# Kernel tuning notes

Measured on AMD Instinct MI355X. Metric: run time of the kernel, lower is better.

## Reference

```python
import jax, jax.numpy as jnp
import numpy as np

N, F, E, B, D = 100000, 256, 128, 10000, 32
GAMMA, ZETA = -0.1, 1.1  # hard-concrete stretch params of L0Dense


def setup_inputs() -> dict:
    key = jax.random.key(0)
    ks = jax.random.split(key, 12)
    return {
        "nodes": jax.random.randint(ks[0], (B,), 0, N),
        "neigh_idx": jax.random.randint(ks[1], (B, D), 0, N),
        "neigh_mask": jax.random.bernoulli(ks[2], 0.9, (B, D)),
        "feature": jax.random.normal(ks[3], (N, F), jnp.float32),
        "W": jax.random.normal(ks[4], (F, E), jnp.float32) * 0.05,
        "b": jnp.zeros((E,), jnp.float32),
        "qz_loga": jax.random.normal(ks[5], (F,), jnp.float32),
        "att1_w": jax.random.normal(ks[6], (2 * E, E), jnp.float32) * 0.05,
        "att1_b": jnp.zeros((E,), jnp.float32),
        "att2_w": jax.random.normal(ks[7], (E, E), jnp.float32) * 0.05,
        "att2_b": jnp.zeros((E,), jnp.float32),
        "att3_w": jax.random.normal(ks[8], (E, 1), jnp.float32) * 0.05,
        "att3_b": jnp.zeros((1,), jnp.float32),
    }


def reference(nodes, neigh_idx, neigh_mask, feature, W, b, qz_loga,
              att1_w, att1_b, att2_w, att2_b, att3_w, att3_b):
    # L0Dense, deterministic (eval) hard-concrete gate on input dims
    z = jnp.clip(jax.nn.sigmoid(qz_loga) * (ZETA - GAMMA) + GAMMA, 0.0, 1.0)
    We = W * z[:, None]                                  # [F, E]

    node_feat = feature[nodes] @ We + b                   # [B, E]
    neigh_feat = feature[neigh_idx] @ We + b              # [B, D, E]

    # GraphRec-style attention MLP over (neighbor, center) pairs
    h = jnp.concatenate(
        [neigh_feat, jnp.broadcast_to(node_feat[:, None, :], neigh_feat.shape)],
        axis=-1)                                          # [B, D, 2E]
    h = jax.nn.relu(h @ att1_w + att1_b)
    h = jax.nn.relu(h @ att2_w + att2_b)
    scores = (h @ att3_w + att3_b)[..., 0]                # [B, D]
    scores = jnp.where(neigh_mask, scores, -1e30)
    att = jax.nn.softmax(scores, axis=-1)                 # [B, D]

    agg = jnp.einsum('bd,bde->be', att, neigh_feat)       # weighted sum
    has_neigh = neigh_mask.any(axis=-1, keepdims=True)
    return jnp.where(has_neigh, agg, node_feat)           # n==0 fallback
```

## Files before the change

### kernel.cpp

```cpp
#include <hip/hip_runtime.h>
#include <hip/hip_bf16.h>
#include <math.h>

#define NN 100000
#define FF 256
#define EE 128
#define BB_ 10000
#define DD 32

typedef __attribute__((ext_vector_type(8))) short short8;
typedef __attribute__((ext_vector_type(4))) float f32x4;

__device__ __forceinline__ short f2bf(float f) {
  __hip_bfloat16 h = __float2bfloat16(f);
  union { __hip_bfloat16 h; short s; } u; u.h = h;
  return u.s;
}
__device__ __forceinline__ float bf2f(short s) {
  union { unsigned u; float f; } v;
  v.u = ((unsigned)(unsigned short)s) << 16;
  return v.f;
}

__device__ __forceinline__ void gll16(const float* g, float* lds) {
  __builtin_amdgcn_global_load_lds(
      (const __attribute__((address_space(1))) unsigned int*)g,
      (__attribute__((address_space(3))) unsigned int*)lds, 16, 0, 0);
}

__global__ __launch_bounds__(256) void k_prep(
    const float* __restrict__ W, const float* __restrict__ qz,
    const float* __restrict__ a1w, const float* __restrict__ a2w,
    const float* __restrict__ bb,
    float* __restrict__ Wef32, short* __restrict__ BT2,
    short* __restrict__ a1wTc, short* __restrict__ w2T,
    float* __restrict__ bias2) {
  int i = blockIdx.x * 256 + threadIdx.x;
  if (i < 32768) {
    int f = i >> 7, e = i & 127;
    float g = qz[f];
    float s = 1.0f / (1.0f + expf(-g));
    float z = fminf(fmaxf(s * 1.2f - 0.1f, 0.0f), 1.0f);
    float v = W[f * 128 + e] * z;
    Wef32[f * 128 + e] = v;
    BT2[e * 256 + f] = f2bf(v);
  } else if (i < 49152) {
    int t = i - 32768; int n = t >> 7, k = t & 127;
    a1wTc[n * 128 + k] = f2bf(a1w[(128 + k) * 128 + n]);
  } else if (i < 65536) {
    int t = i - 49152; int n = t >> 7, k = t & 127;
    w2T[n * 128 + k] = f2bf(a2w[k * 128 + n]);
  } else if (i < 65664) {
    bias2[i - 65536] = bb[i - 65536];
  }
}

__global__ __launch_bounds__(256) void k_compose(
    const float* __restrict__ Wef32, const float* __restrict__ a1w,
    const float* __restrict__ a1b, const float* __restrict__ bb,
    short* __restrict__ BT2, float* __restrict__ bias2) {
  const int n = blockIdx.x;
  const int f = threadIdx.x;
  float s = 0.f;
  for (int e = 0; e < 128; ++e)
    s = fmaf(a1w[e * 128 + n], Wef32[f * 128 + e], s);
  BT2[(size_t)(128 + n) * 256 + f] = f2bf(s);
  if (f == 0) {
    float by = a1b[n];
    for (int e = 0; e < 128; ++e) by = fmaf(bb[e], a1w[e * 128 + n], by);
    bias2[128 + n] = by;
  }
}

__global__ __launch_bounds__(256) void k_xy(
    const float* __restrict__ feat, const short* __restrict__ BT2,
    const float* __restrict__ bias2, short* __restrict__ XY, int M) {
  __shared__ float As[2][32 * 256];
  const int tid = threadIdx.x;
  const int wave = tid >> 6, lane = tid & 63;
  const int wn = wave;
  const int l15 = lane & 15, lg = lane >> 4;
  const int NT = M >> 5;
  const int G = gridDim.x;

  short8 bfr[8][4];
#pragma unroll
  for (int ks = 0; ks < 8; ++ks)
#pragma unroll
    for (int j = 0; j < 4; ++j)
      bfr[ks][j] = *(const short8*)(BT2 +
          (size_t)(wn * 64 + j * 16 + l15) * 256 + (ks * 4 + lg) * 8);
  float bv4[4];
#pragma unroll
  for (int j = 0; j < 4; ++j) bv4[j] = bias2[wn * 64 + j * 16 + l15];

  int t = blockIdx.x;
  if (t < NT) {
#pragma unroll
    for (int it = 0; it < 8; ++it) {
      int r = it * 4 + wave;
      gll16(feat + (size_t)(t * 32 + r) * 256 + ((lane ^ (r & 7)) * 4),
            &As[0][r * 256]);
    }
  }

  int cur = 0;
  for (; t < NT; t += G) {
    const int tn = t + G;
    __builtin_amdgcn_s_barrier();
    if (tn < NT) {
#pragma unroll
      for (int it = 0; it < 8; ++it) {
        int r = it * 4 + wave;
        gll16(feat + (size_t)(tn * 32 + r) * 256 + ((lane ^ (r & 7)) * 4),
              &As[cur ^ 1][r * 256]);
      }
      asm volatile("s_waitcnt vmcnt(8)" ::: "memory");
    } else {
      asm volatile("s_waitcnt vmcnt(0)" ::: "memory");
    }
    __builtin_amdgcn_s_barrier();
    __builtin_amdgcn_sched_barrier(0);

    f32x4 acc[2][4];
#pragma unroll
    for (int i = 0; i < 2; ++i)
#pragma unroll
      for (int j = 0; j < 4; ++j) acc[i][j] = (f32x4){0.f, 0.f, 0.f, 0.f};

    const float* Ab = &As[cur][0];
#pragma unroll
    for (int ks = 0; ks < 8; ++ks) {
      const int kg = ks * 4 + lg;
#pragma unroll
      for (int i = 0; i < 2; ++i) {
        const int r = i * 16 + l15;
        const int sw = r & 7;
        const int c0 = (2 * kg) ^ sw;
        const int c1 = (2 * kg + 1) ^ sw;
        float4 flo = *(const float4*)(Ab + r * 256 + c0 * 4);
        float4 fhi = *(const float4*)(Ab + r * 256 + c1 * 4);
        short8 af;
        af[0] = f2bf(flo.x); af[1] = f2bf(flo.y);
        af[2] = f2bf(flo.z); af[3] = f2bf(flo.w);
        af[4] = f2bf(fhi.x); af[5] = f2bf(fhi.y);
        af[6] = f2bf(fhi.z); af[7] = f2bf(fhi.w);
        __builtin_amdgcn_s_setprio(1);
#pragma unroll
        for (int j = 0; j < 4; ++j)
          acc[i][j] = __builtin_amdgcn_mfma_f32_16x16x32_bf16(
              af, bfr[ks][j], acc[i][j], 0, 0, 0);
        __builtin_amdgcn_s_setprio(0);
      }
    }

#pragma unroll
    for (int i = 0; i < 2; ++i) {
#pragma unroll
      for (int r = 0; r < 4; ++r) {
        int row = t * 32 + i * 16 + lg * 4 + r;
#pragma unroll
        for (int j = 0; j < 4; ++j) {
          int col = wn * 64 + j * 16 + l15;
          XY[(size_t)row * 256 + col] = f2bf(acc[i][j][r] + bv4[j]);
        }
      }
    }
    cur ^= 1;
  }
}

template <int K, int LDA, int LDC, bool AF32, bool OUTBF16>
__global__ __launch_bounds__(256) void k_mm(
    const void* __restrict__ Ap, const short* __restrict__ BT,
    const float* __restrict__ bias, const int* __restrict__ idx,
    void* __restrict__ Cp, int M) {
  __shared__ short As[128 * 64];
  __shared__ short Bs[128 * 64];
  const int tid = threadIdx.x;
  const int mb = blockIdx.x * 128;
  const int col0 = blockIdx.y * 128;
  const int wave = tid >> 6, lane = tid & 63;
  const int wr = wave >> 1, wc = wave & 1;
  const int l15 = lane & 15, lg = lane >> 4;

  size_t abase[4];
#pragma unroll
  for (int s = 0; s < 4; ++s) {
    int row = (tid + s * 256) >> 3;
    int grow = mb + row;
    int gr = 0;
    if (grow < M) gr = idx ? idx[grow] : grow;
    abase[s] = (size_t)gr * LDA;
  }

  f32x4 acc[4][4];
#pragma unroll
  for (int i = 0; i < 4; ++i)
#pragma unroll
    for (int j = 0; j < 4; ++j) acc[i][j] = (f32x4){0.f, 0.f, 0.f, 0.f};

  for (int k0 = 0; k0 < K; k0 += 64) {
#pragma unroll
    for (int s = 0; s < 4; ++s) {
      int q = tid + s * 256;
      int row = q >> 3, c = q & 7;
      short8 av;
      if (AF32) {
        const float* ap = (const float*)Ap + abase[s] + k0 + c * 8;
        float4 f0 = *(const float4*)ap;
        float4 f1 = *(const float4*)(ap + 4);
        av[0] = f2bf(f0.x); av[1] = f2bf(f0.y);
        av[2] = f2bf(f0.z); av[3] = f2bf(f0.w);
        av[4] = f2bf(f1.x); av[5] = f2bf(f1.y);
        av[6] = f2bf(f1.z); av[7] = f2bf(f1.w);
      } else {
        av = *(const short8*)((const short*)Ap + abase[s] + k0 + c * 8);
      }
      *(short8*)(As + row * 64 + 8 * (c ^ (row & 7))) = av;
      short8 bv = *(const short8*)(BT + (size_t)(col0 + row) * K + k0 + c * 8);
      *(short8*)(Bs + row * 64 + 8 * (c ^ (row & 7))) = bv;
    }
    __syncthreads();
#pragma unroll
    for (int ks = 0; ks < 2; ++ks) {
      int c = ks * 4 + lg;
      short8 af[4], bfv[4];
#pragma unroll
      for (int i = 0; i < 4; ++i) {
        int r = wr * 64 + i * 16 + l15;
        af[i] = *(short8*)(As + r * 64 + 8 * (c ^ (r & 7)));
        int n = wc * 64 + i * 16 + l15;
        bfv[i] = *(short8*)(Bs + n * 64 + 8 * (c ^ (n & 7)));
      }
#pragma unroll
      for (int i = 0; i < 4; ++i)
#pragma unroll
        for (int j = 0; j < 4; ++j)
          acc[i][j] = __builtin_amdgcn_mfma_f32_16x16x32_bf16(
              af[i], bfv[j], acc[i][j], 0, 0, 0);
    }
    __syncthreads();
  }

  float bv4[4];
#pragma unroll
  for (int j = 0; j < 4; ++j) {
    int col = wc * 64 + j * 16 + l15;
    bv4[j] = bias ? bias[col0 + col] : 0.f;
  }
#pragma unroll
  for (int i = 0; i < 4; ++i) {
#pragma unroll
    for (int r = 0; r < 4; ++r) {
      int row = mb + wr * 64 + i * 16 + lg * 4 + r;
      if (row < M) {
#pragma unroll
        for (int j = 0; j < 4; ++j) {
          int col = wc * 64 + j * 16 + l15;
          float v = acc[i][j][r] + bv4[j];
          if (OUTBF16)
            ((short*)Cp)[(size_t)row * LDC + col0 + col] = f2bf(v);
          else
            ((float*)Cp)[(size_t)row * LDC + col0 + col] = v;
        }
      }
    }
  }
}

__global__ __launch_bounds__(256) void k_attn6(
    const short* __restrict__ XY, const float* __restrict__ P,
    const int* __restrict__ nodes, const int* __restrict__ nidx,
    const int* __restrict__ nmask, const short* __restrict__ w2T,
    const float* __restrict__ b2, const float* __restrict__ w3,
    const float* __restrict__ b3, float* __restrict__ out) {
  __shared__ float sc_s[4][32];
  __shared__ float att_s[4][32];
  const int tid = threadIdx.x;
  const int wave = tid >> 6, lane = tid & 63;
  const int l15 = lane & 15, lg = lane >> 4;
  const int w0 = blockIdx.x * 4 + wave;
  const float b3v = b3[0];

  float b2v[2][4], w3v[2][4];
#pragma unroll
  for (int cg = 0; cg < 2; ++cg)
#pragma unroll
    for (int j = 0; j < 4; ++j) {
      const int col = cg * 64 + j * 16 + l15;
      b2v[cg][j] = b2[col];
      w3v[cg][j] = w3[col];
    }

  int b = w0;
  int xc = nidx[b * DD + (lane & 31)];
  int mc = nmask[b * DD + (lane & 31)];
  unsigned xfb = *(const unsigned*)(XY + (size_t)nodes[b] * 256 + 2 * lane);
  int nb0 = __shfl(xc, l15), nb1 = __shfl(xc, 16 + l15);
  short8 y0v[4], y1v[4];
#pragma unroll
  for (int ks = 0; ks < 4; ++ks) {
    const int k0 = ks * 32 + lg * 8;
    y0v[ks] = *(const short8*)(XY + (size_t)nb0 * 256 + 128 + k0);
    y1v[ks] = *(const short8*)(XY + (size_t)nb1 * 256 + 128 + k0);
  }
  float4 pv[8];
#pragma unroll
  for (int q = 0; q < 4; ++q) {
    const int k0 = q * 32 + lg * 8;
    pv[2 * q] = *(const float4*)(P + (size_t)b * EE + k0);
    pv[2 * q + 1] = *(const float4*)(P + (size_t)b * EE + k0 + 4);
  }

#pragma unroll 1
  for (int it = 0; it < 4; ++it) {
    const int bn = (it < 3) ? b + 2500 : b;
    int xn = nidx[bn * DD + (lane & 31)];
    int mn = nmask[bn * DD + (lane & 31)];
    unsigned xfbn =
        *(const unsigned*)(XY + (size_t)nodes[bn] * 256 + 2 * lane);

    unsigned xv[32];
#pragma unroll
    for (int d = 0; d < 32; ++d)
      xv[d] = *(const unsigned*)(XY + (size_t)__shfl(xc, d) * 256 + 2 * lane);

    short8 a0[4], a1[4];
#pragma unroll
    for (int ks = 0; ks < 4; ++ks) {
      float pf[8] = {pv[2 * ks].x, pv[2 * ks].y, pv[2 * ks].z, pv[2 * ks].w,
                     pv[2 * ks + 1].x, pv[2 * ks + 1].y, pv[2 * ks + 1].z,
                     pv[2 * ks + 1].w};
#pragma unroll
      for (int e = 0; e < 8; ++e) {
        a0[ks][e] = f2bf(fmaxf(bf2f(y0v[ks][e]) + pf[e], 0.f));
        a1[ks][e] = f2bf(fmaxf(bf2f(y1v[ks][e]) + pf[e], 0.f));
      }
    }

    float sp[2][4];
#pragma unroll
    for (int i = 0; i < 2; ++i)
#pragma unroll
      for (int r = 0; r < 4; ++r) sp[i][r] = 0.f;

#pragma unroll
    for (int cg = 0; cg < 2; ++cg) {
      f32x4 acc[2][4];
#pragma unroll
      for (int i = 0; i < 2; ++i)
#pragma unroll
        for (int j = 0; j < 4; ++j) acc[i][j] = (f32x4){0.f, 0.f, 0.f, 0.f};
#pragma unroll
      for (int ks = 0; ks < 4; ++ks) {
        const int k0 = ks * 32 + lg * 8;
        short8 bfv[4];
#pragma unroll
        for (int j = 0; j < 4; ++j)
          bfv[j] = *(const short8*)(w2T +
              (size_t)(cg * 64 + j * 16 + l15) * EE + k0);
        __builtin_amdgcn_s_setprio(1);
#pragma unroll
        for (int j = 0; j < 4; ++j) {
          acc[0][j] = __builtin_amdgcn_mfma_f32_16x16x32_bf16(
              a0[ks], bfv[j], acc[0][j], 0, 0, 0);
          acc[1][j] = __builtin_amdgcn_mfma_f32_16x16x32_bf16(
              a1[ks], bfv[j], acc[1][j], 0, 0, 0);
        }
        __builtin_amdgcn_s_setprio(0);
      }
      if (cg == 0) {
        const int nb0n = __shfl(xn, l15), nb1n = __shfl(xn, 16 + l15);
#pragma unroll
        for (int ks = 0; ks < 4; ++ks) {
          const int k0 = ks * 32 + lg * 8;
          y0v[ks] = *(const short8*)(XY + (size_t)nb0n * 256 + 128 + k0);
          y1v[ks] = *(const short8*)(XY + (size_t)nb1n * 256 + 128 + k0);
        }
      }
#pragma unroll
      for (int j = 0; j < 4; ++j) {
#pragma unroll
        for (int i = 0; i < 2; ++i)
#pragma unroll
          for (int r = 0; r < 4; ++r)
            sp[i][r] += fmaxf(acc[i][j][r] + b2v[cg][j], 0.f) * w3v[cg][j];
      }
    }

#pragma unroll
    for (int q = 0; q < 4; ++q) {
      const int k0 = q * 32 + lg * 8;
      pv[2 * q] = *(const float4*)(P + (size_t)bn * EE + k0);
      pv[2 * q + 1] = *(const float4*)(P + (size_t)bn * EE + k0 + 4);
    }

#pragma unroll
    for (int off = 1; off <= 8; off <<= 1) {
#pragma unroll
      for (int i = 0; i < 2; ++i)
#pragma unroll
        for (int r = 0; r < 4; ++r) sp[i][r] += __shfl_xor(sp[i][r], off);
    }
    if (l15 == 0) {
#pragma unroll
      for (int i = 0; i < 2; ++i)
#pragma unroll
        for (int r = 0; r < 4; ++r)
          sc_s[wave][i * 16 + lg * 4 + r] = sp[i][r];
    }

    const int row = lane & 31;
    float s = sc_s[wave][row] + b3v;
    if (!mc) s = -1e30f;
    float mx = s;
#pragma unroll
    for (int off = 1; off <= 16; off <<= 1)
      mx = fmaxf(mx, __shfl_xor(mx, off));
    float e = expf(s - mx);
    float sum = e;
#pragma unroll
    for (int off = 1; off <= 16; off <<= 1) sum += __shfl_xor(sum, off);
    if (lane < 32) att_s[wave][row] = e / sum;
    const bool has = (__ballot(mc != 0) != 0ull);

    float a0f = 0.f, a1f = 0.f;
    if (has) {
#pragma unroll
      for (int d = 0; d < 32; ++d) {
        const float a = att_s[wave][d];
        a0f += a * bf2f((short)(xv[d] & 0xffffu));
        a1f += a * bf2f((short)(xv[d] >> 16));
      }
    } else {
      a0f = bf2f((short)(xfb & 0xffffu));
      a1f = bf2f((short)(xfb >> 16));
    }
    *(float2*)(out + (size_t)b * EE + 2 * lane) = make_float2(a0f, a1f);

    xc = xn; mc = mn; xfb = xfbn; b = bn;
  }
}

extern "C" void kernel_launch(void* const* d_in, const int* in_sizes, int n_in,
                              void* d_out, int out_size, void* d_ws,
                              size_t ws_size, hipStream_t stream) {
  const int* nodes = (const int*)d_in[0];
  const int* nidx = (const int*)d_in[1];
  const int* nmask = (const int*)d_in[2];
  const float* feature = (const float*)d_in[3];
  const float* W = (const float*)d_in[4];
  const float* bb = (const float*)d_in[5];
  const float* qz = (const float*)d_in[6];
  const float* a1w = (const float*)d_in[7];
  const float* a1b = (const float*)d_in[8];
  const float* a2w = (const float*)d_in[9];
  const float* a2b = (const float*)d_in[10];
  const float* a3w = (const float*)d_in[11];
  const float* a3b = (const float*)d_in[12];
  float* out = (float*)d_out;

  char* ws = (char*)d_ws;
  short* BT2   = (short*)(ws);
  float* Wef32 = (float*)(ws + 131072);
  short* a1wTc = (short*)(ws + 262144);
  short* w2T   = (short*)(ws + 294912);
  float* bias2 = (float*)(ws + 327680);
  short* XYb   = (short*)(ws + 524288);
  float* Pv    = (float*)(ws + 524288 + 51200000);

  k_prep<<<257, 256, 0, stream>>>(W, qz, a1w, a2w, bb, Wef32, BT2, a1wTc, w2T,
                                  bias2);
  k_compose<<<128, 256, 0, stream>>>(Wef32, a1w, a1b, bb, BT2, bias2);
  k_xy<<<512, 256, 0, stream>>>(feature, BT2, bias2, XYb, NN);
  k_mm<128, 256, 128, false, false><<<dim3((BB_ + 127) / 128, 1), 256, 0,
                                      stream>>>(XYb, a1wTc, nullptr, nodes, Pv,
                                                BB_);
  k_attn6<<<625, 256, 0, stream>>>(XYb, Pv, nodes, nidx, nmask, w2T, a2b,
                                   a3w, a3b, out);
}
```

Baseline: 123.0 us.

## Process two batch rows per wave in one pass instead of a 4-iteration loop

The attention kernel used to run 625 blocks, and each wave looped over 4 batch rows, prefetching the next row's data while computing the current one. Now each wave handles two adjacent batch rows at once across 1250 blocks. The two rows' MFMAs are interleaved so they share each w2T B-fragment load, and both softmaxes are done together using the two 32-lane halves of the wave. This gives more parallelism and more memory-level parallelism at the cost of more registers per wave, which may lower occupancy, and it drops the cross-iteration software prefetch.

```diff
diff --git a/kernel.cpp b/kernel.cpp
--- a/kernel.cpp
+++ b/kernel.cpp
@@ -269,178 +269,217 @@
   }
 }
 
-__global__ __launch_bounds__(256) void k_attn6(
+__global__ __launch_bounds__(256) void k_attn7(
     const short* __restrict__ XY, const float* __restrict__ P,
     const int* __restrict__ nodes, const int* __restrict__ nidx,
     const int* __restrict__ nmask, const short* __restrict__ w2T,
     const float* __restrict__ b2, const float* __restrict__ w3,
     const float* __restrict__ b3, float* __restrict__ out) {
-  __shared__ float sc_s[4][32];
-  __shared__ float att_s[4][32];
+  __shared__ float sc_s[4][2][32];
+  __shared__ float att_s[4][2][32];
   const int tid = threadIdx.x;
   const int wave = tid >> 6, lane = tid & 63;
   const int l15 = lane & 15, lg = lane >> 4;
-  const int w0 = blockIdx.x * 4 + wave;
+  const int dl = lane & 31;
+  const int b0 = (blockIdx.x * 4 + wave) * 2;
+  const int b1 = b0 + 1;
   const float b3v = b3[0];
 
-  float b2v[2][4], w3v[2][4];
+  float b2h[2][4], w3h[2][4];
 #pragma unroll
   for (int cg = 0; cg < 2; ++cg)
 #pragma unroll
     for (int j = 0; j < 4; ++j) {
       const int col = cg * 64 + j * 16 + l15;
-      b2v[cg][j] = b2[col];
-      w3v[cg][j] = w3[col];
-    }
-
-  int b = w0;
-  int xc = nidx[b * DD + (lane & 31)];
-  int mc = nmask[b * DD + (lane & 31)];
-  unsigned xfb = *(const unsigned*)(XY + (size_t)nodes[b] * 256 + 2 * lane);
-  int nb0 = __shfl(xc, l15), nb1 = __shfl(xc, 16 + l15);
-  short8 y0v[4], y1v[4];
+      b2h[cg][j] = b2[col];
+      w3h[cg][j] = w3[col];
+    }
+
+  const int ni0 = nidx[b0 * DD + dl];
+  const int ni1 = nidx[b1 * DD + dl];
+  const int m0 = nmask[b0 * DD + dl];
+  const int m1 = nmask[b1 * DD + dl];
+  const unsigned xfb0 =
+      *(const unsigned*)(XY + (size_t)nodes[b0] * 256 + 2 * lane);
+  const unsigned xfb1 =
+      *(const unsigned*)(XY + (size_t)nodes[b1] * 256 + 2 * lane);
+
+  const int r00 = __shfl(ni0, l15), r01 = __shfl(ni0, 16 + l15);
+  const int r10 = __shfl(ni1, l15), r11 = __shfl(ni1, 16 + l15);
+
+  short8 y00[4], y01[4], y10[4], y11[4];
 #pragma unroll
   for (int ks = 0; ks < 4; ++ks) {
     const int k0 = ks * 32 + lg * 8;
-    y0v[ks] = *(const short8*)(XY + (size_t)nb0 * 256 + 128 + k0);
-    y1v[ks] = *(const short8*)(XY + (size_t)nb1 * 256 + 128 + k0);
+    y00[ks] = *(const short8*)(XY + (size_t)r00 * 256 + 128 + k0);
+    y01[ks] = *(const short8*)(XY + (size_t)r01 * 256 + 128 + k0);
+    y10[ks] = *(const short8*)(XY + (size_t)r10 * 256 + 128 + k0);
+    y11[ks] = *(const short8*)(XY + (size_t)r11 * 256 + 128 + k0);
   }
   float4 pv[8];
 #pragma unroll
   for (int q = 0; q < 4; ++q) {
     const int k0 = q * 32 + lg * 8;
-    pv[2 * q] = *(const float4*)(P + (size_t)b * EE + k0);
-    pv[2 * q + 1] = *(const float4*)(P + (size_t)b * EE + k0 + 4);
-  }
-
-#pragma unroll 1
-  for (int it = 0; it < 4; ++it) {
-    const int bn = (it < 3) ? b + 2500 : b;
-    int xn = nidx[bn * DD + (lane & 31)];
-    int mn = nmask[bn * DD + (lane & 31)];
-    unsigned xfbn =
-        *(const unsigned*)(XY + (size_t)nodes[bn] * 256 + 2 * lane);
-
-    unsigned xv[32];
-#pragma unroll
-    for (int d = 0; d < 32; ++d)
-      xv[d] = *(const unsigned*)(XY + (size_t)__shfl(xc, d) * 256 + 2 * lane);
-
-    short8 a0[4], a1[4];
+    pv[2 * q] = *(const float4*)(P + (size_t)b0 * EE + k0);
+    pv[2 * q + 1] = *(const float4*)(P + (size_t)b0 * EE + k0 + 4);
+  }
+
+  short8 f00[4], f01[4];
+#pragma unroll
+  for (int ks = 0; ks < 4; ++ks) {
+    float pf[8] = {pv[2 * ks].x, pv[2 * ks].y, pv[2 * ks].z, pv[2 * ks].w,
+                   pv[2 * ks + 1].x, pv[2 * ks + 1].y, pv[2 * ks + 1].z,
+                   pv[2 * ks + 1].w};
+#pragma unroll
+    for (int e = 0; e < 8; ++e) {
+      f00[ks][e] = f2bf(fmaxf(bf2f(y00[ks][e]) + pf[e], 0.f));
+      f01[ks][e] = f2bf(fmaxf(bf2f(y01[ks][e]) + pf[e], 0.f));
+    }
+  }
+
+#pragma unroll
+  for (int q = 0; q < 4; ++q) {
+    const int k0 = q * 32 + lg * 8;
+    pv[2 * q] = *(const float4*)(P + (size_t)b1 * EE + k0);
+    pv[2 * q + 1] = *(const float4*)(P + (size_t)b1 * EE + k0 + 4);
+  }
+  unsigned xv0[32];
+#pragma unroll
+  for (int d = 0; d < 32; ++d)
+    xv0[d] = *(const unsigned*)(XY + (size_t)__shfl(ni0, d) * 256 + 2 * lane);
+
+  short8 f10[4], f11[4];
+#pragma unroll
+  for (int ks = 0; ks < 4; ++ks) {
+    float pf[8] = {pv[2 * ks].x, pv[2 * ks].y, pv[2 * ks].z, pv[2 * ks].w,
+                   pv[2 * ks + 1].x, pv[2 * ks + 1].y, pv[2 * ks + 1].z,
+                   pv[2 * ks + 1].w};
+#pragma unroll
+    for (int e = 0; e < 8; ++e) {
+      f10[ks][e] = f2bf(fmaxf(bf2f(y10[ks][e]) + pf[e], 0.f));
+      f11[ks][e] = f2bf(fmaxf(bf2f(y11[ks][e]) + pf[e], 0.f));
+    }
+  }
+
+  float sp0[2][4], sp1[2][4];
+#pragma unroll
+  for (int i = 0; i < 2; ++i)
+#pragma unroll
+    for (int r = 0; r < 4; ++r) { sp0[i][r] = 0.f; sp1[i][r] = 0.f; }
+
+#pragma unroll
+  for (int cg = 0; cg < 2; ++cg) {
+    f32x4 ac0[2][4], ac1[2][4];
+#pragma unroll
+    for (int i = 0; i < 2; ++i)
+#pragma unroll
+      for (int j = 0; j < 4; ++j) {
+        ac0[i][j] = (f32x4){0.f, 0.f, 0.f, 0.f};
+        ac1[i][j] = (f32x4){0.f, 0.f, 0.f, 0.f};
+      }
 #pragma unroll
     for (int ks = 0; ks < 4; ++ks) {
-      float pf[8] = {pv[2 * ks].x, pv[2 * ks].y, pv[2 * ks].z, pv[2 * ks].w,
-                     pv[2 * ks + 1].x, pv[2 * ks + 1].y, pv[2 * ks + 1].z,
-                     pv[2 * ks + 1].w};
-#pragma unroll
-      for (int e = 0; e < 8; ++e) {
-        a0[ks][e] = f2bf(fmaxf(bf2f(y0v[ks][e]) + pf[e], 0.f));
-        a1[ks][e] = f2bf(fmaxf(bf2f(y1v[ks][e]) + pf[e], 0.f));
-      }
-    }
-
-    float sp[2][4];
+      const int k0 = ks * 32 + lg * 8;
+      short8 bfv[4];
+#pragma unroll
+      for (int j = 0; j < 4; ++j)
+        bfv[j] = *(const short8*)(w2T +
+            (size_t)(cg * 64 + j * 16 + l15) * EE + k0);
+      __builtin_amdgcn_s_setprio(1);
+#pragma unroll
+      for (int j = 0; j < 4; ++j) {
+        ac0[0][j] = __builtin_amdgcn_mfma_f32_16x16x32_bf16(
+            f00[ks], bfv[j], ac0[0][j], 0, 0, 0);
+        ac0[1][j] = __builtin_amdgcn_mfma_f32_16x16x32_bf16(
+            f01[ks], bfv[j], ac0[1][j], 0, 0, 0);
+        ac1[0][j] = __builtin_amdgcn_mfma_f32_16x16x32_bf16(
+            f10[ks], bfv[j], ac1[0][j], 0, 0, 0);
+        ac1[1][j] = __builtin_amdgcn_mfma_f32_16x16x32_bf16(
+            f11[ks], bfv[j], ac1[1][j], 0, 0, 0);
+      }
+      __builtin_amdgcn_s_setprio(0);
+    }
+#pragma unroll
+    for (int j = 0; j < 4; ++j) {
+#pragma unroll
+      for (int i = 0; i < 2; ++i)
+#pragma unroll
+        for (int r = 0; r < 4; ++r) {
+          sp0[i][r] += fmaxf(ac0[i][j][r] + b2h[cg][j], 0.f) * w3h[cg][j];
+          sp1[i][r] += fmaxf(ac1[i][j][r] + b2h[cg][j], 0.f) * w3h[cg][j];
+        }
+    }
+  }
+
+  unsigned xv1[32];
+#pragma unroll
+  for (int d = 0; d < 32; ++d)
+    xv1[d] = *(const unsigned*)(XY + (size_t)__shfl(ni1, d) * 256 + 2 * lane);
+
+#pragma unroll
+  for (int off = 1; off <= 8; off <<= 1) {
 #pragma unroll
     for (int i = 0; i < 2; ++i)
 #pragma unroll
-      for (int r = 0; r < 4; ++r) sp[i][r] = 0.f;
-
-#pragma unroll
-    for (int cg = 0; cg < 2; ++cg) {
-      f32x4 acc[2][4];
-#pragma unroll
-      for (int i = 0; i < 2; ++i)
-#pragma unroll
-        for (int j = 0; j < 4; ++j) acc[i][j] = (f32x4){0.f, 0.f, 0.f, 0.f};
-#pragma unroll
-      for (int ks = 0; ks < 4; ++ks) {
-        const int k0 = ks * 32 + lg * 8;
-        short8 bfv[4];
-#pragma unroll
-        for (int j = 0; j < 4; ++j)
-          bfv[j] = *(const short8*)(w2T +
-              (size_t)(cg * 64 + j * 16 + l15) * EE + k0);
-        __builtin_amdgcn_s_setprio(1);
-#pragma unroll
-        for (int j = 0; j < 4; ++j) {
-          acc[0][j] = __builtin_amdgcn_mfma_f32_16x16x32_bf16(
-              a0[ks], bfv[j], acc[0][j], 0, 0, 0);
-          acc[1][j] = __builtin_amdgcn_mfma_f32_16x16x32_bf16(
-              a1[ks], bfv[j], acc[1][j], 0, 0, 0);
-        }
-        __builtin_amdgcn_s_setprio(0);
-      }
-      if (cg == 0) {
-        const int nb0n = __shfl(xn, l15), nb1n = __shfl(xn, 16 + l15);
-#pragma unroll
-        for (int ks = 0; ks < 4; ++ks) {
-          const int k0 = ks * 32 + lg * 8;
-          y0v[ks] = *(const short8*)(XY + (size_t)nb0n * 256 + 128 + k0);
-          y1v[ks] = *(const short8*)(XY + (size_t)nb1n * 256 + 128 + k0);
-        }
-      }
-#pragma unroll
-      for (int j = 0; j < 4; ++j) {
-#pragma unroll
-        for (int i = 0; i < 2; ++i)
-#pragma unroll
-          for (int r = 0; r < 4; ++r)
-            sp[i][r] += fmaxf(acc[i][j][r] + b2v[cg][j], 0.f) * w3v[cg][j];
-      }
-    }
-
-#pragma unroll
-    for (int q = 0; q < 4; ++q) {
-      const int k0 = q * 32 + lg * 8;
-      pv[2 * q] = *(const float4*)(P + (size_t)bn * EE + k0);
-      pv[2 * q + 1] = *(const float4*)(P + (size_t)bn * EE + k0 + 4);
-    }
-
-#pragma unroll
-    for (int off = 1; off <= 8; off <<= 1) {
-#pragma unroll
-      for (int i = 0; i < 2; ++i)
-#pragma unroll
-        for (int r = 0; r < 4; ++r) sp[i][r] += __shfl_xor(sp[i][r], off);
-    }
-    if (l15 == 0) {
-#pragma unroll
-      for (int i = 0; i < 2; ++i)
-#pragma unroll
-        for (int r = 0; r < 4; ++r)
-          sc_s[wave][i * 16 + lg * 4 + r] = sp[i][r];
-    }
-
-    const int row = lane & 31;
-    float s = sc_s[wave][row] + b3v;
-    if (!mc) s = -1e30f;
-    float mx = s;
-#pragma unroll
-    for (int off = 1; off <= 16; off <<= 1)
-      mx = fmaxf(mx, __shfl_xor(mx, off));
-    float e = expf(s - mx);
-    float sum = e;
-#pragma unroll
-    for (int off = 1; off <= 16; off <<= 1) sum += __shfl_xor(sum, off);
-    if (lane < 32) att_s[wave][row] = e / sum;
-    const bool has = (__ballot(mc != 0) != 0ull);
-
-    float a0f = 0.f, a1f = 0.f;
-    if (has) {
-#pragma unroll
-      for (int d = 0; d < 32; ++d) {
-        const float a = att_s[wave][d];
-        a0f += a * bf2f((short)(xv[d] & 0xffffu));
-        a1f += a * bf2f((short)(xv[d] >> 16));
-      }
-    } else {
-      a0f = bf2f((short)(xfb & 0xffffu));
-      a1f = bf2f((short)(xfb >> 16));
-    }
-    *(float2*)(out + (size_t)b * EE + 2 * lane) = make_float2(a0f, a1f);
-
-    xc = xn; mc = mn; xfb = xfbn; b = bn;
-  }
+      for (int r = 0; r < 4; ++r) {
+        sp0[i][r] += __shfl_xor(sp0[i][r], off);
+        sp1[i][r] += __shfl_xor(sp1[i][r], off);
+      }
+  }
+  if (l15 == 0) {
+#pragma unroll
+    for (int i = 0; i < 2; ++i)
+#pragma unroll
+      for (int r = 0; r < 4; ++r) {
+        sc_s[wave][0][i * 16 + lg * 4 + r] = sp0[i][r];
+        sc_s[wave][1][i * 16 + lg * 4 + r] = sp1[i][r];
+      }
+  }
+
+  const int half = lane >> 5;
+  const int row = dl;
+  const int mh = half ? m1 : m0;
+  float s = sc_s[wave][half][row] + b3v;
+  if (!mh) s = -1e30f;
+  float mx = s;
+#pragma unroll
+  for (int off = 1; off <= 16; off <<= 1) mx = fmaxf(mx, __shfl_xor(mx, off));
+  float e = expf(s - mx);
+  float sum = e;
+#pragma unroll
+  for (int off = 1; off <= 16; off <<= 1) sum += __shfl_xor(sum, off);
+  att_s[wave][half][row] = e / sum;
+  const unsigned long long bal = __ballot(mh != 0);
+  const bool has0 = (bal & 0xffffffffull) != 0ull;
+  const bool has1 = (bal >> 32) != 0ull;
+
+  float a00 = 0.f, a01 = 0.f;
+  if (has0) {
+#pragma unroll
+    for (int d = 0; d < 32; ++d) {
+      const float a = att_s[wave][0][d];
+      a00 += a * bf2f((short)(xv0[d] & 0xffffu));
+      a01 += a * bf2f((short)(xv0[d] >> 16));
+    }
+  } else {
+    a00 = bf2f((short)(xfb0 & 0xffffu));
+    a01 = bf2f((short)(xfb0 >> 16));
+  }
+  *(float2*)(out + (size_t)b0 * EE + 2 * lane) = make_float2(a00, a01);
+
+  float a10 = 0.f, a11 = 0.f;
+  if (has1) {
+#pragma unroll
+    for (int d = 0; d < 32; ++d) {
+      const float a = att_s[wave][1][d];
+      a10 += a * bf2f((short)(xv1[d] & 0xffffu));
+      a11 += a * bf2f((short)(xv1[d] >> 16));
+    }
+  } else {
+    a10 = bf2f((short)(xfb1 & 0xffffu));
+    a11 = bf2f((short)(xfb1 >> 16));
+  }
+  *(float2*)(out + (size_t)b1 * EE + 2 * lane) = make_float2(a10, a11);
 }
 
 extern "C" void kernel_launch(void* const* d_in, const int* in_sizes, int n_in,
@@ -477,6 +516,6 @@
   k_mm<128, 256, 128, false, false><<<dim3((BB_ + 127) / 128, 1), 256, 0,
                                       stream>>>(XYb, a1wTc, nullptr, nodes, Pv,
                                                 BB_);
-  k_attn6<<<625, 256, 0, stream>>>(XYb, Pv, nodes, nidx, nmask, w2T, a2b,
-                                   a3w, a3b, out);
-}
+  k_attn7<<<BB_ / 8, 256, 0, stream>>>(XYb, Pv, nodes, nidx, nmask, w2T, a2b,
+                                       a3w, a3b, out);
+}
```

Result: faster. 113.4 us, median of 2 (-7.8%).
